# Kernel tuning notes

Hardware: AMD Instinct MI355X
Metric: run time of the kernel (lower is better)

## Reference

```python
import jax, jax.numpy as jnp
import numpy as np

N_NODES = 50000
N_EDGES = 800000
N_GRAPHS = 512
VOCAB = 128
HID = 64
NCLS = 5


def _seg_mean(vals, ids, num_segments):
    s = jax.ops.segment_sum(vals, ids, num_segments=num_segments)
    cnt = jax.ops.segment_sum(jnp.ones((vals.shape[0],), vals.dtype), ids, num_segments=num_segments)
    return s / jnp.maximum(cnt, 1.0)[:, None]


def sage_conv(x, src, dst, W_l, b_l, W_r):
    # PyG SAGEConv (mean aggr): out = lin_l(mean_{j in N(i)} x_j) + lin_r(x_i)
    agg = _seg_mean(x[src], dst, x.shape[0])          # [N, H] gather + scatter-mean
    return agg @ W_l.T + b_l + x @ W_r.T


def setup_inputs() -> dict:
    key = jax.random.key(0)
    ks = jax.random.split(key, 10)
    scale = 1.0 / np.sqrt(HID)
    x_tokens = jax.random.randint(ks[0], (N_NODES,), 0, VOCAB)
    edge_index = jax.random.randint(ks[1], (2, N_EDGES), 0, N_NODES)
    batch = jnp.sort(jax.random.randint(ks[2], (N_NODES,), 0, N_GRAPHS))
    return {
        "x_tokens": x_tokens,
        "edge_index": edge_index,
        "batch": batch,
        "embed": jax.random.normal(ks[3], (VOCAB, HID), jnp.float32),
        "W1l": jax.random.normal(ks[4], (HID, HID), jnp.float32) * scale,
        "b1l": jnp.zeros((HID,), jnp.float32),
        "W1r": jax.random.normal(ks[5], (HID, HID), jnp.float32) * scale,
        "W2l": jax.random.normal(ks[6], (HID, HID), jnp.float32) * scale,
        "b2l": jnp.zeros((HID,), jnp.float32),
        "W2r": jax.random.normal(ks[7], (HID, HID), jnp.float32) * scale,
        "Wlin": jax.random.normal(ks[8], (NCLS, HID), jnp.float32) * scale,
        "blin": jnp.zeros((NCLS,), jnp.float32),
    }


def reference(x_tokens, edge_index, batch, embed, W1l, b1l, W1r, W2l, b2l, W2r, Wlin, blin):
    src, dst = edge_index[0], edge_index[1]
    x = embed[x_tokens]                                  # [N, H] embedding lookup
    x = jax.nn.relu(sage_conv(x, src, dst, W1l, b1l, W1r))
    x = jax.nn.relu(sage_conv(x, src, dst, W2l, b2l, W2r))
    g = _seg_mean(x, batch, N_GRAPHS)                    # global_mean_pool -> [G, H]
    return g @ Wlin.T + blin                             # [G, num_classes]
```

## Files before the change

kernel.cpp:

```cpp
#include <hip/hip_runtime.h>

#define N_NODES  50000
#define N_EDGES  800000
#define N_GRAPHS 512
#define HID      64
#define NCLS     5
#define NB       64
#define EST      36
#define AST      68

typedef __attribute__((ext_vector_type(8))) short bf16x8;
typedef __attribute__((ext_vector_type(4))) float f32x4;

__device__ inline unsigned short f2bf(float f) {
    unsigned int u = __builtin_bit_cast(unsigned int, f);
    unsigned int r = (u + 0x7FFFu + ((u >> 16) & 1u)) >> 16;
    return (unsigned short)r;
}
__device__ inline unsigned int packbf(float a, float b) {
    return (unsigned int)f2bf(a) | ((unsigned int)f2bf(b) << 16);
}
__device__ inline float bf2f(unsigned int u16) {
    unsigned int t = u16 << 16;
    return __builtin_bit_cast(float, t);
}

#define XCDS   8
#define NPX    (N_NODES / XCDS)
#define EPB    512
#define ECH2   ((N_EDGES + EPB - 1) / EPB)
#define SEC_E  (ECH2 * XCDS * 256)
#define EBUF_T (128 * 32)
#define PW_T   (64 * 64)
#define PREP_T (SEC_E + EBUF_T + N_NODES + 2 * PW_T)
__global__ void k_prep_fill(
    const int* __restrict__ src, const int* __restrict__ dst,
    const int* __restrict__ tok,
    int* __restrict__ cnt, unsigned int* __restrict__ bucket,
    const float* __restrict__ embed, unsigned int* __restrict__ ebufg,
    const int* __restrict__ batch,
    int* __restrict__ pos_start, int* __restrict__ pos_end,
    const float* __restrict__ W1l, const float* __restrict__ W1r,
    unsigned int* __restrict__ wb1,
    const float* __restrict__ W2l, const float* __restrict__ W2r,
    unsigned int* __restrict__ wb2) {
    int gid = blockIdx.x * blockDim.x + threadIdx.x;
    if (gid < SEC_E) {
        int blk   = gid >> 8;
        int tidl  = gid & 255;
        int range = blk & 7;
        int chunk = blk >> 3;
        int lo = range * NPX;
        int e0 = chunk * EPB + tidl;
        int e1 = e0 + 256;
        int d0 = (e0 < N_EDGES) ? dst[e0] : -1;
        int d1 = (e1 < N_EDGES) ? dst[e1] : -1;
        int s0 = (e0 < N_EDGES) ? src[e0] : 0;
        int s1 = (e1 < N_EDGES) ? src[e1] : 0;
        bool k0 = (d0 >= lo) && (d0 < lo + NPX);
        bool k1 = (d1 >= lo) && (d1 < lo + NPX);
        unsigned int t0 = k0 ? (unsigned int)tok[s0] : 0u;
        unsigned int t1 = k1 ? (unsigned int)tok[s1] : 0u;
        if (k0) {
            int pos = atomicAdd(&cnt[d0], 1);
            if (pos < NB) bucket[(long)d0 * NB + pos] = (unsigned int)s0 | (t0 << 16);
        }
        if (k1) {
            int pos = atomicAdd(&cnt[d1], 1);
            if (pos < NB) bucket[(long)d1 * NB + pos] = (unsigned int)s1 | (t1 << 16);
        }
        return;
    }
    gid -= SEC_E;
    if (gid < EBUF_T) {
        int t = gid >> 5, c = gid & 31;
        float2 v = ((const float2*)(embed + (long)t * HID))[c];
        ebufg[gid] = packbf(v.x, v.y);
        return;
    }
    gid -= EBUF_T;
    if (gid < N_NODES) {
        int n = gid;
        int b = batch[n];
        if (n == 0 || batch[n - 1] != b) pos_start[b] = n;
        if (n == N_NODES - 1 || batch[n + 1] != b) pos_end[b] = n + 1;
        return;
    }
    gid -= N_NODES;
    if (gid < 2 * PW_T) {
        const float* Wl = (gid < PW_T) ? W1l : W2l;
        const float* Wr = (gid < PW_T) ? W1r : W2r;
        unsigned int* wb = (gid < PW_T) ? wb1 : wb2;
        int i = (gid < PW_T) ? gid : gid - PW_T;
        int h = i >> 6, c = i & 63;
        float2 v = (c < 32) ? ((const float2*)(Wl + (long)h * HID))[c]
                            : ((const float2*)(Wr + (long)h * HID))[c - 32];
        wb[i] = packbf(v.x, v.y);
    }
}

template <bool L1, int NPBT>
__global__ __launch_bounds__(NPBT * 16) void k_layer(
    const int* __restrict__ cnt, const unsigned int* __restrict__ bucket,
    const int* __restrict__ tok, const unsigned int* __restrict__ ebufg,
    const unsigned int* __restrict__ xb,
    const unsigned int* __restrict__ wb, const float* __restrict__ bl,
    unsigned short* __restrict__ xoutb,
    const int* __restrict__ batch, float* __restrict__ gacc)
{
    __shared__ unsigned int As[NPBT * AST];
    __shared__ unsigned int elds[L1 ? 128 * EST : 1];
    const int tid  = threadIdx.x;
    const int wv   = tid >> 6;
    const int lane = tid & 63;
    const int n0   = blockIdx.x * NPBT;

    if (L1) {
        for (int i = tid; i < EBUF_T; i += NPBT * 16) {
            int t = i >> 5, c = i & 31;
            elds[t * EST + c] = ebufg[i];
        }
        __syncthreads();
    }

    const int q  = lane & 7;
    const int e8 = lane >> 3;

    int degA[4]; unsigned int vA[4]; int mA[4]; int ncA[4];
#pragma unroll
    for (int i = 0; i < 4; ++i) {
        int nn = n0 + wv * 4 + i;
        int nc = min(nn, N_NODES - 1);
        ncA[i] = nc;
        degA[i] = cnt[nc];
        vA[i] = bucket[(long)nc * NB + lane];
    }
#pragma unroll
    for (int i = 0; i < 4; ++i) {
        int nn = n0 + wv * 4 + i;
        mA[i] = (nn < N_NODES) ? min(degA[i], NB) : 0;
    }

#pragma unroll
    for (int i = 0; i < 4; ++i) {
        int rl = wv * 4 + i;
        int m  = mA[i];
        uint4 w4[8];
#pragma unroll
        for (int g = 0; g < 8; ++g) {
            int j = g * 8 + e8;
            unsigned int vv = __shfl(vA[i], j, 64);
            vv = (j < m) ? vv : 0u;
            if (L1) w4[g] = *(const uint4*)(elds + (vv >> 16) * EST + q * 4);
            else    w4[g] = *((const uint4*)(xb + (long)(vv & 0xffffu) * 32) + q);
        }
        float f0 = 0, f1 = 0, f2 = 0, f3 = 0, f4 = 0, f5 = 0, f6 = 0, f7 = 0;
#pragma unroll
        for (int g = 0; g < 8; ++g) {
            int j = g * 8 + e8;
            if (j < m) {
                f0 += bf2f(w4[g].x & 0xffff); f1 += bf2f(w4[g].x >> 16);
                f2 += bf2f(w4[g].y & 0xffff); f3 += bf2f(w4[g].y >> 16);
                f4 += bf2f(w4[g].z & 0xffff); f5 += bf2f(w4[g].z >> 16);
                f6 += bf2f(w4[g].w & 0xffff); f7 += bf2f(w4[g].w >> 16);
            }
        }
#pragma unroll
        for (int o = 8; o < 64; o <<= 1) {
            f0 += __shfl_xor(f0, o, 64); f1 += __shfl_xor(f1, o, 64);
            f2 += __shfl_xor(f2, o, 64); f3 += __shfl_xor(f3, o, 64);
            f4 += __shfl_xor(f4, o, 64); f5 += __shfl_xor(f5, o, 64);
            f6 += __shfl_xor(f6, o, 64); f7 += __shfl_xor(f7, o, 64);
        }
        if (e8 == 0) {
            float inv = 1.0f / (float)max(degA[i], 1);
            uint4 o;
            o.x = packbf(f0 * inv, f1 * inv);
            o.y = packbf(f2 * inv, f3 * inv);
            o.z = packbf(f4 * inv, f5 * inv);
            o.w = packbf(f6 * inv, f7 * inv);
            *(uint4*)(As + rl * AST + q * 4) = o;
        } else if (e8 == 1) {
            uint4 sv;
            if (L1) { int tk = tok[ncA[i]]; sv = *(const uint4*)(elds + tk * EST + q * 4); }
            else    { sv = *((const uint4*)(xb + (long)ncA[i] * 32) + q); }
            *(uint4*)(As + rl * AST + 32 + q * 4) = sv;
        }
    }
    __syncthreads();

    constexpr int NSTR = NPBT / 16;
    const int s    = wv % NSTR;
    const int t    = wv / NSTR;
    const int mm   = lane & 15;
    const int quad = lane >> 4;

    bf16x8 afr[4];
#pragma unroll
    for (int kst = 0; kst < 4; ++kst)
        afr[kst] = *(const bf16x8*)(As + (s * 16 + mm) * AST + kst * 16 + quad * 4);

    f32x4 acc = (f32x4){0.f, 0.f, 0.f, 0.f};
#pragma unroll
    for (int kst = 0; kst < 4; ++kst) {
        bf16x8 bfr = *(const bf16x8*)(wb + (t * 16 + mm) * 64 + kst * 16 + quad * 4);
        acc = __builtin_amdgcn_mfma_f32_16x16x32_bf16(bfr, afr[kst], acc, 0, 0, 0);
    }

    int node = n0 + s * 16 + mm;
    int hb = t * 16 + quad * 4;
    float4 bb = *(const float4*)(bl + hb);
    float a0 = fmaxf(acc[0] + bb.x, 0.f);
    float a1 = fmaxf(acc[1] + bb.y, 0.f);
    float a2 = fmaxf(acc[2] + bb.z, 0.f);
    float a3 = fmaxf(acc[3] + bb.w, 0.f);

    if constexpr (L1) {
        if (node < N_NODES) {
            ushort4 o;
            o.x = f2bf(a0); o.y = f2bf(a1); o.z = f2bf(a2); o.w = f2bf(a3);
            *(ushort4*)(xoutb + (long)node * HID + hb) = o;
        }
    } else {
        int g = batch[node];
#pragma unroll
        for (int off = 1; off < 16; off <<= 1) {
            float o0 = __shfl_up(a0, off, 16), o1 = __shfl_up(a1, off, 16);
            float o2 = __shfl_up(a2, off, 16), o3 = __shfl_up(a3, off, 16);
            int   og = __shfl_up(g, off, 16);
            if (mm >= off && og == g) { a0 += o0; a1 += o1; a2 += o2; a3 += o3; }
        }
        int gn = __shfl_down(g, 1, 16);
        if (mm == 15 || gn != g) {
            float* dp = gacc + g * HID + hb;
            unsafeAtomicAdd(dp + 0, a0);
            unsafeAtomicAdd(dp + 1, a1);
            unsafeAtomicAdd(dp + 2, a2);
            unsafeAtomicAdd(dp + 3, a3);
        }
    }
}

__global__ __launch_bounds__(256) void k_head(
    const float* __restrict__ gacc,
    const int* __restrict__ pstart, const int* __restrict__ pend,
    const float* __restrict__ Wlin, const float* __restrict__ blin,
    float* __restrict__ out)
{
    int g = blockIdx.x * blockDim.x + threadIdx.x;
    if (g >= N_GRAPHS) return;
    float inv = 1.0f / (float)max(pend[g] - pstart[g], 1);
    float s0 = 0, s1 = 0, s2 = 0, s3 = 0, s4 = 0;
    const float* row = gacc + g * HID;
#pragma unroll 8
    for (int k = 0; k < HID; ++k) {
        float mk = row[k] * inv;
        s0 += mk * Wlin[0 * HID + k];
        s1 += mk * Wlin[1 * HID + k];
        s2 += mk * Wlin[2 * HID + k];
        s3 += mk * Wlin[3 * HID + k];
        s4 += mk * Wlin[4 * HID + k];
    }
    out[g * NCLS + 0] = s0 + blin[0];
    out[g * NCLS + 1] = s1 + blin[1];
    out[g * NCLS + 2] = s2 + blin[2];
    out[g * NCLS + 3] = s3 + blin[3];
    out[g * NCLS + 4] = s4 + blin[4];
}

extern "C" void kernel_launch(void* const* d_in, const int* in_sizes, int n_in,
                              void* d_out, int out_size, void* d_ws, size_t ws_size,
                              hipStream_t stream) {
    const int*   tok   = (const int*)d_in[0];
    const int*   eidx  = (const int*)d_in[1];
    const int*   batch = (const int*)d_in[2];
    const float* embed = (const float*)d_in[3];
    const float* W1l   = (const float*)d_in[4];
    const float* b1l   = (const float*)d_in[5];
    const float* W1r   = (const float*)d_in[6];
    const float* W2l   = (const float*)d_in[7];
    const float* b2l   = (const float*)d_in[8];
    const float* W2r   = (const float*)d_in[9];
    const float* Wlin  = (const float*)d_in[10];
    const float* blin  = (const float*)d_in[11];
    float* out = (float*)d_out;

    const int* src = eidx;
    const int* dst = eidx + N_EDGES;

    char* wsp = (char*)d_ws;
    size_t off = 0;
    auto alloc = [&](size_t bytes) -> void* {
        void* p = wsp + off;
        off = (off + bytes + 255) & ~(size_t)255;
        return p;
    };
    int*   cnt     = (int*)  alloc((size_t)N_NODES * 4);
    int*   pstart  = (int*)  alloc((size_t)N_GRAPHS * 4);
    int*   pend    = (int*)  alloc((size_t)N_GRAPHS * 4);
    float* gacc    = (float*)alloc((size_t)N_GRAPHS * HID * 4);
    unsigned int* bucket = (unsigned int*)alloc((size_t)N_NODES * NB * 4);
    unsigned int* x1b    = (unsigned int*)alloc((size_t)N_NODES * 32 * 4);
    unsigned int* ebufg  = (unsigned int*)alloc((size_t)128 * 32 * 4);
    unsigned int* wb1    = (unsigned int*)alloc((size_t)64 * 64 * 4);
    unsigned int* wb2    = (unsigned int*)alloc((size_t)64 * 64 * 4);

    hipMemsetAsync(cnt, 0, ((char*)gacc + (size_t)N_GRAPHS * HID * 4) - (char*)cnt, stream);

    k_prep_fill<<<(PREP_T + 255) / 256, 256, 0, stream>>>(
        src, dst, tok, cnt, bucket,
        embed, ebufg, batch, pstart, pend, W1l, W1r, wb1, W2l, W2r, wb2);

    k_layer<true, 32><<<(N_NODES + 31) / 32, 512, 0, stream>>>(
        cnt, bucket, tok, ebufg, nullptr, wb1, b1l, (unsigned short*)x1b,
        nullptr, nullptr);
    k_layer<false, 16><<<N_NODES / 16, 256, 0, stream>>>(
        cnt, bucket, nullptr, nullptr, x1b, wb2, b2l, nullptr,
        batch, gacc);

    k_head<<<(N_GRAPHS + 255) / 256, 256, 0, stream>>>(
        gacc, pstart, pend, Wlin, blin, out);
}
```

Measured before the change: 191.2 us.

## Precompute embed projections so layer 1 skips the matmul

Because layer-1 input is an embedding lookup over 128 tokens, the linear maps are applied to the embedding table first (embed·W1lᵀ and embed·W1rᵀ), and layer 1 becomes a mean over gathered precomputed rows plus a self row, bias and ReLU, with no MFMA stage or LDS staging. This removes the per-node layer-1 matmul and the sync around it, at the cost of a small extra dot-product pass in the prep kernel and twice the LDS table size. Rounding changes slightly because the aggregation now runs over bf16 projected values instead of bf16 embeddings.

New measurement: 185.0 us. 1.03x faster.

```diff
diff --git a/kernel.cpp b/kernel.cpp
--- a/kernel.cpp
+++ b/kernel.cpp
@@ -30,18 +30,18 @@
 #define EPB    512
 #define ECH2   ((N_EDGES + EPB - 1) / EPB)
 #define SEC_E  (ECH2 * XCDS * 256)
-#define EBUF_T (128 * 32)
+#define E_T    (2 * 128 * 32)
 #define PW_T   (64 * 64)
-#define PREP_T (SEC_E + EBUF_T + N_NODES + 2 * PW_T)
+#define PREP_T (SEC_E + E_T + N_NODES + PW_T)
 __global__ void k_prep_fill(
     const int* __restrict__ src, const int* __restrict__ dst,
     const int* __restrict__ tok,
     int* __restrict__ cnt, unsigned int* __restrict__ bucket,
-    const float* __restrict__ embed, unsigned int* __restrict__ ebufg,
+    const float* __restrict__ embed,
+    const float* __restrict__ W1l, const float* __restrict__ W1r,
+    unsigned int* __restrict__ e1g,
     const int* __restrict__ batch,
     int* __restrict__ pos_start, int* __restrict__ pos_end,
-    const float* __restrict__ W1l, const float* __restrict__ W1r,
-    unsigned int* __restrict__ wb1,
     const float* __restrict__ W2l, const float* __restrict__ W2r,
     unsigned int* __restrict__ wb2) {
     int gid = blockIdx.x * blockDim.x + threadIdx.x;
@@ -72,13 +72,24 @@
         return;
     }
     gid -= SEC_E;
-    if (gid < EBUF_T) {
-        int t = gid >> 5, c = gid & 31;
-        float2 v = ((const float2*)(embed + (long)t * HID))[c];
-        ebufg[gid] = packbf(v.x, v.y);
+    if (gid < E_T) {
+        int idx = gid & 4095;
+        int t = idx >> 5, c = idx & 31;
+        const float* W = (gid < 4096) ? W1l : W1r;
+        const float* e  = embed + (long)t * HID;
+        const float* w0 = W + (long)(2 * c) * HID;
+        const float* w1 = w0 + HID;
+        float a0 = 0.f, a1 = 0.f;
+#pragma unroll 8
+        for (int k = 0; k < HID; ++k) {
+            float ev = e[k];
+            a0 += ev * w0[k];
+            a1 += ev * w1[k];
+        }
+        e1g[gid] = packbf(a0, a1);
         return;
     }
-    gid -= EBUF_T;
+    gid -= E_T;
     if (gid < N_NODES) {
         int n = gid;
         int b = batch[n];
@@ -87,41 +98,100 @@
         return;
     }
     gid -= N_NODES;
-    if (gid < 2 * PW_T) {
-        const float* Wl = (gid < PW_T) ? W1l : W2l;
-        const float* Wr = (gid < PW_T) ? W1r : W2r;
-        unsigned int* wb = (gid < PW_T) ? wb1 : wb2;
-        int i = (gid < PW_T) ? gid : gid - PW_T;
-        int h = i >> 6, c = i & 63;
-        float2 v = (c < 32) ? ((const float2*)(Wl + (long)h * HID))[c]
-                            : ((const float2*)(Wr + (long)h * HID))[c - 32];
-        wb[i] = packbf(v.x, v.y);
-    }
-}
-
-template <bool L1, int NPBT>
-__global__ __launch_bounds__(NPBT * 16) void k_layer(
+    if (gid < PW_T) {
+        int h = gid >> 6, c = gid & 63;
+        float2 v = (c < 32) ? ((const float2*)(W2l + (long)h * HID))[c]
+                            : ((const float2*)(W2r + (long)h * HID))[c - 32];
+        wb2[gid] = packbf(v.x, v.y);
+    }
+}
+
+__global__ __launch_bounds__(512) void k_layer1(
     const int* __restrict__ cnt, const unsigned int* __restrict__ bucket,
-    const int* __restrict__ tok, const unsigned int* __restrict__ ebufg,
-    const unsigned int* __restrict__ xb,
-    const unsigned int* __restrict__ wb, const float* __restrict__ bl,
-    unsigned short* __restrict__ xoutb,
-    const int* __restrict__ batch, float* __restrict__ gacc)
+    const int* __restrict__ tok, const unsigned int* __restrict__ e1g,
+    const float* __restrict__ bl, unsigned int* __restrict__ x1b)
 {
-    __shared__ unsigned int As[NPBT * AST];
-    __shared__ unsigned int elds[L1 ? 128 * EST : 1];
+    __shared__ unsigned int el[128 * EST];
+    __shared__ unsigned int er[128 * EST];
     const int tid  = threadIdx.x;
     const int wv   = tid >> 6;
     const int lane = tid & 63;
-    const int n0   = blockIdx.x * NPBT;
-
-    if (L1) {
-        for (int i = tid; i < EBUF_T; i += NPBT * 16) {
-            int t = i >> 5, c = i & 31;
-            elds[t * EST + c] = ebufg[i];
-        }
-        __syncthreads();
-    }
+    const int n0   = blockIdx.x * 32;
+
+    for (int i = tid; i < 4096; i += 512) {
+        int t = i >> 5, c = i & 31;
+        el[t * EST + c] = e1g[i];
+        er[t * EST + c] = e1g[4096 + i];
+    }
+    __syncthreads();
+
+    const int q  = lane & 7;
+    const int e8 = lane >> 3;
+
+    int degA[4]; unsigned int vA[4]; int tkA[4];
+#pragma unroll
+    for (int i = 0; i < 4; ++i) {
+        int nn = n0 + wv * 4 + i;
+        int nc = min(nn, N_NODES - 1);
+        degA[i] = cnt[nc];
+        vA[i]   = bucket[(long)nc * NB + lane];
+        tkA[i]  = tok[nc];
+    }
+
+#pragma unroll
+    for (int i = 0; i < 4; ++i) {
+        int nn = n0 + wv * 4 + i;
+        int m  = (nn < N_NODES) ? min(degA[i], NB) : 0;
+        float f0 = 0, f1 = 0, f2 = 0, f3 = 0, f4 = 0, f5 = 0, f6 = 0, f7 = 0;
+#pragma unroll
+        for (int g = 0; g < 8; ++g) {
+            int j = g * 8 + e8;
+            unsigned int vv = __shfl(vA[i], j, 64);
+            if (j < m) {
+                uint4 w4 = *(const uint4*)(el + (vv >> 16) * EST + q * 4);
+                f0 += bf2f(w4.x & 0xffff); f1 += bf2f(w4.x >> 16);
+                f2 += bf2f(w4.y & 0xffff); f3 += bf2f(w4.y >> 16);
+                f4 += bf2f(w4.z & 0xffff); f5 += bf2f(w4.z >> 16);
+                f6 += bf2f(w4.w & 0xffff); f7 += bf2f(w4.w >> 16);
+            }
+        }
+#pragma unroll
+        for (int o = 8; o < 64; o <<= 1) {
+            f0 += __shfl_xor(f0, o, 64); f1 += __shfl_xor(f1, o, 64);
+            f2 += __shfl_xor(f2, o, 64); f3 += __shfl_xor(f3, o, 64);
+            f4 += __shfl_xor(f4, o, 64); f5 += __shfl_xor(f5, o, 64);
+            f6 += __shfl_xor(f6, o, 64); f7 += __shfl_xor(f7, o, 64);
+        }
+        if (e8 == 0 && nn < N_NODES) {
+            float inv = 1.0f / (float)max(degA[i], 1);
+            uint4 sv = *(const uint4*)(er + tkA[i] * EST + q * 4);
+            float4 b0 = *(const float4*)(bl + q * 8);
+            float4 b1 = *(const float4*)(bl + q * 8 + 4);
+            uint4 o;
+            o.x = packbf(fmaxf(f0 * inv + bf2f(sv.x & 0xffff) + b0.x, 0.f),
+                         fmaxf(f1 * inv + bf2f(sv.x >> 16)    + b0.y, 0.f));
+            o.y = packbf(fmaxf(f2 * inv + bf2f(sv.y & 0xffff) + b0.z, 0.f),
+                         fmaxf(f3 * inv + bf2f(sv.y >> 16)    + b0.w, 0.f));
+            o.z = packbf(fmaxf(f4 * inv + bf2f(sv.z & 0xffff) + b1.x, 0.f),
+                         fmaxf(f5 * inv + bf2f(sv.z >> 16)    + b1.y, 0.f));
+            o.w = packbf(fmaxf(f6 * inv + bf2f(sv.w & 0xffff) + b1.z, 0.f),
+                         fmaxf(f7 * inv + bf2f(sv.w >> 16)    + b1.w, 0.f));
+            *(uint4*)(x1b + (long)nn * 32 + q * 4) = o;
+        }
+    }
+}
+
+__global__ __launch_bounds__(256) void k_layer2(
+    const int* __restrict__ cnt, const unsigned int* __restrict__ bucket,
+    const unsigned int* __restrict__ xb,
+    const unsigned int* __restrict__ wb, const float* __restrict__ bl,
+    const int* __restrict__ batch, float* __restrict__ gacc)
+{
+    __shared__ unsigned int As[16 * AST];
+    const int tid  = threadIdx.x;
+    const int wv   = tid >> 6;
+    const int lane = tid & 63;
+    const int n0   = blockIdx.x * 16;
 
     const int q  = lane & 7;
     const int e8 = lane >> 3;
@@ -151,8 +221,7 @@
             int j = g * 8 + e8;
             unsigned int vv = __shfl(vA[i], j, 64);
             vv = (j < m) ? vv : 0u;
-            if (L1) w4[g] = *(const uint4*)(elds + (vv >> 16) * EST + q * 4);
-            else    w4[g] = *((const uint4*)(xb + (long)(vv & 0xffffu) * 32) + q);
+            w4[g] = *((const uint4*)(xb + (long)(vv & 0xffffu) * 32) + q);
         }
         float f0 = 0, f1 = 0, f2 = 0, f3 = 0, f4 = 0, f5 = 0, f6 = 0, f7 = 0;
 #pragma unroll
@@ -181,24 +250,20 @@
             o.w = packbf(f6 * inv, f7 * inv);
             *(uint4*)(As + rl * AST + q * 4) = o;
         } else if (e8 == 1) {
-            uint4 sv;
-            if (L1) { int tk = tok[ncA[i]]; sv = *(const uint4*)(elds + tk * EST + q * 4); }
-            else    { sv = *((const uint4*)(xb + (long)ncA[i] * 32) + q); }
+            uint4 sv = *((const uint4*)(xb + (long)ncA[i] * 32) + q);
             *(uint4*)(As + rl * AST + 32 + q * 4) = sv;
         }
     }
     __syncthreads();
 
-    constexpr int NSTR = NPBT / 16;
-    const int s    = wv % NSTR;
-    const int t    = wv / NSTR;
+    const int t    = wv;
     const int mm   = lane & 15;
     const int quad = lane >> 4;
 
     bf16x8 afr[4];
 #pragma unroll
     for (int kst = 0; kst < 4; ++kst)
-        afr[kst] = *(const bf16x8*)(As + (s * 16 + mm) * AST + kst * 16 + quad * 4);
+        afr[kst] = *(const bf16x8*)(As + mm * AST + kst * 16 + quad * 4);
 
     f32x4 acc = (f32x4){0.f, 0.f, 0.f, 0.f};
 #pragma unroll
@@ -207,7 +272,7 @@
         acc = __builtin_amdgcn_mfma_f32_16x16x32_bf16(bfr, afr[kst], acc, 0, 0, 0);
     }
 
-    int node = n0 + s * 16 + mm;
+    int node = n0 + mm;
     int hb = t * 16 + quad * 4;
     float4 bb = *(const float4*)(bl + hb);
     float a0 = fmaxf(acc[0] + bb.x, 0.f);
@@ -215,29 +280,21 @@
     float a2 = fmaxf(acc[2] + bb.z, 0.f);
     float a3 = fmaxf(acc[3] + bb.w, 0.f);
 
-    if constexpr (L1) {
-        if (node < N_NODES) {
-            ushort4 o;
-            o.x = f2bf(a0); o.y = f2bf(a1); o.z = f2bf(a2); o.w = f2bf(a3);
-            *(ushort4*)(xoutb + (long)node * HID + hb) = o;
-        }
-    } else {
-        int g = batch[node];
-#pragma unroll
-        for (int off = 1; off < 16; off <<= 1) {
-            float o0 = __shfl_up(a0, off, 16), o1 = __shfl_up(a1, off, 16);
-            float o2 = __shfl_up(a2, off, 16), o3 = __shfl_up(a3, off, 16);
-            int   og = __shfl_up(g, off, 16);
-            if (mm >= off && og == g) { a0 += o0; a1 += o1; a2 += o2; a3 += o3; }
-        }
-        int gn = __shfl_down(g, 1, 16);
-        if (mm == 15 || gn != g) {
-            float* dp = gacc + g * HID + hb;
-            unsafeAtomicAdd(dp + 0, a0);
-            unsafeAtomicAdd(dp + 1, a1);
-            unsafeAtomicAdd(dp + 2, a2);
-            unsafeAtomicAdd(dp + 3, a3);
-        }
+    int g = batch[node];
+#pragma unroll
+    for (int off = 1; off < 16; off <<= 1) {
+        float o0 = __shfl_up(a0, off, 16), o1 = __shfl_up(a1, off, 16);
+        float o2 = __shfl_up(a2, off, 16), o3 = __shfl_up(a3, off, 16);
+        int   og = __shfl_up(g, off, 16);
+        if (mm >= off && og == g) { a0 += o0; a1 += o1; a2 += o2; a3 += o3; }
+    }
+    int gn = __shfl_down(g, 1, 16);
+    if (mm == 15 || gn != g) {
+        float* dp = gacc + g * HID + hb;
+        unsafeAtomicAdd(dp + 0, a0);
+        unsafeAtomicAdd(dp + 1, a1);
+        unsafeAtomicAdd(dp + 2, a2);
+        unsafeAtomicAdd(dp + 3, a3);
     }
 }
 
@@ -301,22 +358,19 @@
     float* gacc    = (float*)alloc((size_t)N_GRAPHS * HID * 4);
     unsigned int* bucket = (unsigned int*)alloc((size_t)N_NODES * NB * 4);
     unsigned int* x1b    = (unsigned int*)alloc((size_t)N_NODES * 32 * 4);
-    unsigned int* ebufg  = (unsigned int*)alloc((size_t)128 * 32 * 4);
-    unsigned int* wb1    = (unsigned int*)alloc((size_t)64 * 64 * 4);
-    unsigned int* wb2    = (unsigned int*)alloc((size_t)64 * 64 * 4);
+    unsigned int* e1g    = (unsigned int*)alloc((size_t)E_T * 4);
+    unsigned int* wb2    = (unsigned int*)alloc((size_t)PW_T * 4);
 
     hipMemsetAsync(cnt, 0, ((char*)gacc + (size_t)N_GRAPHS * HID * 4) - (char*)cnt, stream);
 
     k_prep_fill<<<(PREP_T + 255) / 256, 256, 0, stream>>>(
         src, dst, tok, cnt, bucket,
-        embed, ebufg, batch, pstart, pend, W1l, W1r, wb1, W2l, W2r, wb2);
-
-    k_layer<true, 32><<<(N_NODES + 31) / 32, 512, 0, stream>>>(
-        cnt, bucket, tok, ebufg, nullptr, wb1, b1l, (unsigned short*)x1b,
-        nullptr, nullptr);
-    k_layer<false, 16><<<N_NODES / 16, 256, 0, stream>>>(
-        cnt, bucket, nullptr, nullptr, x1b, wb2, b2l, nullptr,
-        batch, gacc);
+        embed, W1l, W1r, e1g, batch, pstart, pend, W2l, W2r, wb2);
+
+    k_layer1<<<(N_NODES + 31) / 32, 512, 0, stream>>>(
+        cnt, bucket, tok, e1g, b1l, x1b);
+    k_layer2<<<N_NODES / 16, 256, 0, stream>>>(
+        cnt, bucket, x1b, wb2, b2l, batch, gacc);
 
     k_head<<<(N_GRAPHS + 255) / 256, 256, 0, stream>>>(
         gacc, pstart, pend, Wlin, blin, out);
```
